# Kernel tuning notes

Hardware: AMD Instinct MI355X
Metric: run time of the kernel (lower is better)

## Reference

```python
import jax, jax.numpy as jnp
import numpy as np

# ---- static configuration matching init_kwargs ----
SEG = 2                 # segment_size hard-coded in the module
MUL0, MUL1 = 256, 128   # irreps = 256x0e + 128x1o
G = MUL1 // SEG         # 64 groups of 2x1o
INV_DIM = MUL0 + 3 * G  # 448 scalars (0e) after concat with channel_mix
N_IRREPS = INV_DIM + MUL1 + G + 3 * G  # 832 total irreps after regroup
N_NODES = 32768
EPS = 1e-6
_ISQ2 = 1.0 / np.sqrt(2.0)
_ISQ3 = 1.0 / np.sqrt(3.0)
_ISQ6 = 1.0 / np.sqrt(6.0)


def _cg_l2(a, b):
    """CG contraction 1 x 1 -> 2: project a_i b_j onto the 5 orthonormal
    symmetric-traceless basis matrices. a, b: [..., 3] -> [..., 5]."""
    ax, ay, az = a[..., 0], a[..., 1], a[..., 2]
    bx, by, bz = b[..., 0], b[..., 1], b[..., 2]
    return jnp.stack([
        (ax * by + ay * bx) * _ISQ2,
        (ax * bz + az * bx) * _ISQ2,
        (ay * bz + az * by) * _ISQ2,
        (ax * bx - ay * by) * _ISQ2,
        (2 * az * bz - ax * bx - ay * by) * _ISQ6,
    ], axis=-1)


def setup_inputs() -> dict:
    key = jax.random.key(0)
    k = jax.random.split(key, 5)
    return {
        "x":   jax.random.normal(k[0], (N_NODES, MUL0 + 3 * MUL1), dtype=jnp.float32),
        "W1":  jax.random.normal(k[1], (INV_DIM, INV_DIM),   dtype=jnp.float32),
        "W2":  jax.random.normal(k[2], (INV_DIM, N_IRREPS),  dtype=jnp.float32),
        "Wl0": jax.random.normal(k[3], (INV_DIM, MUL0),      dtype=jnp.float32),
        "Wl1": jax.random.normal(k[4], (MUL1, MUL1),         dtype=jnp.float32),
    }


def reference(x, W1, W2, Wl0, Wl1):
    N = x.shape[0]
    dt = x.dtype
    s = x[:, :MUL0]                       # [N, 256]  0e features
    v = x[:, MUL0:].reshape(N, MUL1, 3)   # [N, 128, 3]  1o features

    # ---- segmented tensor_square: groups of 2x1o -> 3x0e + 1x1e + 3x2e ----
    vg = v.reshape(N, G, SEG, 3)
    a, b = vg[:, :, 0], vg[:, :, 1]
    sq2 = jnp.sqrt(jnp.asarray(2.0, dt))
    # 0e: symmetric pairs (0,0), (0,1)*sqrt2, (1,1); CG = delta_ij/sqrt3
    t0 = jnp.stack([(a * a).sum(-1), sq2 * (a * b).sum(-1), (b * b).sum(-1)], -1) * _ISQ3  # [N,G,3]
    # 1e: antisymmetric pair (0,1); CG = eps/sqrt2, pair factor sqrt2 -> plain cross
    t1 = jnp.cross(a, b)                                                                   # [N,G,3]
    # 2e: symmetric pairs
    t2 = jnp.stack([_cg_l2(a, a), sq2 * _cg_l2(a, b), _cg_l2(b, b)], 2)                    # [N,G,3,5]

    # ---- concatenate + regroup (axis_to_mul folds group axis into mul) ----
    s_all = jnp.concatenate([s, t0.reshape(N, 3 * G)], -1)  # [N,448]  448x0e
    v1o = v                                                 # [N,128,3] 128x1o
    v1e = t1                                                # [N,64,3]   64x1e
    v2e = t2.reshape(N, 3 * G, 5)                           # [N,192,5] 192x2e

    # ---- gating MLP on invariants: [448 -> 448 (silu) -> 832] ----
    inv_fan = jnp.sqrt(jnp.asarray(INV_DIM, dt))
    h = jax.nn.silu(s_all @ W1 / inv_fan)
    gates = h @ W2 / inv_fan                                # [N, 832] one scalar per irrep
    g0, g1o, g1e, g2e = jnp.split(gates, [INV_DIM, INV_DIM + MUL1, INV_DIM + MUL1 + G], -1)
    s_all = s_all * g0
    v1o = v1o * g1o[..., None]
    # (v1e * g1e, v2e * g2e are dropped by the Linear below -> omitted, output identical)
    del v1e, v2e, g1e, g2e

    # ---- e3nn Linear to output irreps 256x0e + 128x1o (1e, 2e have no output) ----
    o0 = s_all @ Wl0 / inv_fan                                                   # [N,256]
    o1 = jnp.einsum('nmi,mk->nki', v1o, Wl1) / jnp.sqrt(jnp.asarray(MUL1, dt))   # [N,128,3]

    # ---- equivariant layer norm ----
    mu = o0.mean(-1, keepdims=True)
    var = ((o0 - mu) ** 2).mean(-1, keepdims=True)
    o0 = (o0 - mu) * jax.lax.rsqrt(var + EPS)
    rms = jnp.sqrt((o1 ** 2).mean((-2, -1), keepdims=True) + EPS)
    o1 = o1 / rms

    return jnp.concatenate([o0, o1.reshape(N, 3 * MUL1)], -1)  # [N, 640]
```

## Files before the change

kernel.cpp:

```cpp
#include <hip/hip_runtime.h>
#include <math.h>


typedef float floatx4 __attribute__((ext_vector_type(4)));
typedef __bf16 bf16x8 __attribute__((ext_vector_type(8)));

__device__ __forceinline__ unsigned short f2bf(float f) {
    union { float f; unsigned u; } v; v.f = f;
    unsigned r = v.u + 0x7FFFu + ((v.u >> 16) & 1u);
    return (unsigned short)(r >> 16);
}
__device__ __forceinline__ float bf2f(unsigned short u) {
    union { unsigned u; float f; } v; v.u = ((unsigned)u) << 16; return v.f;
}

__global__ __launch_bounds__(256) void wcast_kernel(
    const float* __restrict__ W1, const float* __restrict__ W2,
    const float* __restrict__ Wl0, const float* __restrict__ Wl1,
    unsigned short* __restrict__ W1F, unsigned short* __restrict__ W2F,
    unsigned short* __restrict__ Wl0F, unsigned short* __restrict__ Wl1F)
{
    int idx = blockIdx.x * 256 + threadIdx.x;
    if (idx < 200704) {
        int e = idx & 7, lane = (idx >> 3) & 63, r2 = idx >> 9;
        int kc = r2 % 14, t = r2 / 14;
        int col = t * 16 + (lane & 15);
        int k   = kc * 32 + (lane >> 4) * 8 + e;
        W1F[idx] = f2bf(W1[k * 448 + col]);
    } else if (idx < 458752) {
        int r = idx - 200704;
        int e = r & 7, lane = (r >> 3) & 63, r2 = r >> 9;
        int kc = r2 % 14, t = r2 / 14;
        int col = t * 16 + (lane & 15);
        int k   = kc * 32 + (lane >> 4) * 8 + e;
        W2F[r] = f2bf(W2[k * 832 + col]);
    } else if (idx < 573440) {
        int r = idx - 458752;
        int e = r & 7, lane = (r >> 3) & 63, r2 = r >> 9;
        int kc = r2 % 14, t = r2 / 14;
        int col = t * 16 + (lane & 15);
        int k   = kc * 32 + (lane >> 4) * 8 + e;
        Wl0F[r] = f2bf(Wl0[k * 256 + col]);
    } else if (idx < 589824) {
        int r = idx - 573440;
        int e = r & 7, lane = (r >> 3) & 63, r2 = r >> 9;
        int kc = r2 % 4, t = r2 / 4;
        int col = t * 16 + (lane & 15);
        int k   = kc * 32 + (lane >> 4) * 8 + e;
        Wl1F[r] = f2bf(Wl1[k * 128 + col]);
    }
}

template<int MT, int NT, int NKC>
__device__ __forceinline__ void gemm_stream(
    const unsigned short* __restrict__ BF, const int tileBase,
    const unsigned short* __restrict__ Albs, const int ldsA, const int rowBase,
    const int lane, const int l15, const int quad, const int wn,
    floatx4 (&acc)[MT][NT])
{
    const unsigned short* bp[NT];
    #pragma unroll
    for (int j = 0; j < NT; ++j)
        bp[j] = BF + ((size_t)(tileBase + wn + 4 * j) * NKC * 64 + lane) * 8;
    #pragma unroll
    for (int kc = 0; kc < NKC; ++kc) {
        bf16x8 af[MT];
        #pragma unroll
        for (int mt = 0; mt < MT; ++mt)
            af[mt] = *(const bf16x8*)&Albs[(rowBase + mt * 16 + l15) * ldsA + kc * 32 + quad * 8];
        #pragma unroll
        for (int j = 0; j < NT; ++j) {
            bf16x8 bfv = *(const bf16x8*)(bp[j] + kc * 512);
            #pragma unroll
            for (int mt = 0; mt < MT; ++mt)
                acc[mt][j] = __builtin_amdgcn_mfma_f32_16x16x32_bf16(af[mt], bfv, acc[mt][j], 0, 0, 0);
        }
    }
}

__global__ __launch_bounds__(512, 2) void fused_kernel(
    const float* __restrict__ x,
    const unsigned short* __restrict__ W1F,
    const unsigned short* __restrict__ W2F,
    const unsigned short* __restrict__ Wl0F,
    const unsigned short* __restrict__ Wl1F,
    float* __restrict__ out)
{
    __shared__ unsigned short sa[64][472];
    __shared__ unsigned short hb[64][472];
    __shared__ unsigned short g1[64][128];
    __shared__ float red[832];

    const int tid  = threadIdx.x;
    const int lane = tid & 63;
    const int l15  = lane & 15;
    const int quad = lane >> 4;
    const int w    = tid >> 6;
    const int wm   = w >> 2;
    const int wn   = w & 3;
    const int n0   = blockIdx.x * 64;

    const float s1 = 0.047245559f;
    const float s2 = 0.088388348f;

    {
        const int r = tid >> 3, sub = tid & 7;
        const float* xr = x + (size_t)(n0 + r) * 640;
        #pragma unroll
        for (int i = 0; i < 8; ++i) {
            int c4 = i * 8 + sub;
            float4 f = *(const float4*)(xr + c4 * 4);
            uint2 p;
            p.x = (unsigned)f2bf(f.x) | ((unsigned)f2bf(f.y) << 16);
            p.y = (unsigned)f2bf(f.z) | ((unsigned)f2bf(f.w) << 16);
            *(uint2*)&sa[r][c4 * 4] = p;
        }
        const float* xv = xr + 256;
        #pragma unroll
        for (int i = 0; i < 8; ++i) {
            int g = i * 8 + sub;
            const float2* vg = (const float2*)(xv + 6 * g);
            float2 p0 = vg[0], p1 = vg[1], p2 = vg[2];
            float ax = p0.x, ay = p0.y, az = p1.x;
            float bx = p1.y, by = p2.x, bz = p2.y;
            float aa = ax*ax + ay*ay + az*az;
            float ab = ax*bx + ay*by + az*bz;
            float bb = bx*bx + by*by + bz*bz;
            const float ISQ3 = 0.57735026918962576f;
            const float SQ2  = 1.41421356237309505f;
            sa[r][256 + 3*g]     = f2bf(aa * ISQ3);
            sa[r][256 + 3*g + 1] = f2bf(SQ2 * ab * ISQ3);
            sa[r][256 + 3*g + 2] = f2bf(bb * ISQ3);
        }
    }
    __syncthreads();

    {
        floatx4 acc[2][7] = {};
        gemm_stream<2,7,14>(W1F, 0, &sa[0][0], 472, wm*32, lane, l15, quad, wn, acc);
        #pragma unroll
        for (int j = 0; j < 7; ++j) {
            const int col = (wn + 4*j) * 16 + l15;
            #pragma unroll
            for (int mt = 0; mt < 2; ++mt)
                #pragma unroll
                for (int r = 0; r < 4; ++r) {
                    float v = acc[mt][j][r] * s1;
                    v = v / (1.f + __expf(-v));
                    hb[wm*32 + mt*16 + quad*4 + r][col] = f2bf(v);
                }
        }
    }
    __syncthreads();

    {
        floatx4 acc[2][9] = {};
        gemm_stream<2,9,14>(W2F, 0, &hb[0][0], 472, wm*32, lane, l15, quad, wn, acc);
        __syncthreads();
        #pragma unroll
        for (int j = 0; j < 9; ++j) {
            const int colb = (wn + 4*j) * 16;
            if (colb < 448) {
                const int col = colb + l15;
                #pragma unroll
                for (int mt = 0; mt < 2; ++mt)
                    #pragma unroll
                    for (int r = 0; r < 4; ++r) {
                        const int row = wm*32 + mt*16 + quad*4 + r;
                        hb[row][col] = f2bf(bf2f(sa[row][col]) * (acc[mt][j][r] * s1));
                    }
            } else {
                const int m = colb - 448 + l15;
                #pragma unroll
                for (int mt = 0; mt < 2; ++mt)
                    #pragma unroll
                    for (int r = 0; r < 4; ++r) {
                        const int row = wm*32 + mt*16 + quad*4 + r;
                        g1[row][m] = f2bf(acc[mt][j][r] * s1);
                    }
            }
        }
    }
    __syncthreads();

    {
        unsigned short* wmp = &sa[0][0];
        #pragma unroll
        for (int e0 = 0; e0 < 6144; e0 += 512) {
            int e4 = e0 + tid;
            int rl = e4 / 96;
            int c4 = (e4 - rl * 96) * 4;
            float4 xv = *(const float4*)(x + (size_t)(n0 + rl) * 640 + 256 + c4);
            float vv[4] = {xv.x, xv.y, xv.z, xv.w};
            #pragma unroll
            for (int d = 0; d < 4; ++d) {
                int rem = c4 + d;
                int m = rem / 3;
                int i = rem - 3 * m;
                wmp[(rl * 3 + i) * 136 + m] = f2bf(vv[d] * bf2f(g1[rl][m]));
            }
        }
    }
    __syncthreads();

    {
        floatx4 acc[2][4] = {};
        gemm_stream<2,4,14>(Wl0F, 0, &hb[0][0], 472, wm*32, lane, l15, quad, wn, acc);
        #pragma unroll
        for (int mt = 0; mt < 2; ++mt)
            #pragma unroll
            for (int r = 0; r < 4; ++r) {
                float sv = 0.f, sq = 0.f;
                #pragma unroll
                for (int j = 0; j < 4; ++j) {
                    float v = acc[mt][j][r] * s1;
                    sv += v; sq += v * v;
                }
                #pragma unroll
                for (int off = 1; off <= 8; off <<= 1) {
                    sv += __shfl_xor(sv, off);
                    sq += __shfl_xor(sq, off);
                }
                if (l15 == 0) {
                    const int row = wm*32 + mt*16 + quad*4 + r;
                    red[row * 8 + wn * 2]     = sv;
                    red[row * 8 + wn * 2 + 1] = sq;
                }
            }
        __syncthreads();
        #pragma unroll
        for (int mt = 0; mt < 2; ++mt)
            #pragma unroll
            for (int r = 0; r < 4; ++r) {
                const int row = wm*32 + mt*16 + quad*4 + r;
                float ts = red[row*8+0] + red[row*8+2] + red[row*8+4] + red[row*8+6];
                float tq = red[row*8+1] + red[row*8+3] + red[row*8+5] + red[row*8+7];
                float mu  = ts * (1.f/256.f);
                float var = tq * (1.f/256.f) - mu * mu;
                float rln = rsqrtf(var + 1e-6f);
                float* orow = out + (size_t)(n0 + row) * 640;
                #pragma unroll
                for (int j = 0; j < 4; ++j)
                    orow[(wn + 4*j)*16 + l15] = (acc[mt][j][r] * s1 - mu) * rln;
            }
    }
    __syncthreads();

    {
        floatx4 acc[6][2] = {};
        gemm_stream<6,2,4>(Wl1F, 0, &sa[0][0] , 136, wm*96, lane, l15, quad, wn, acc);
        #pragma unroll
        for (int mt = 0; mt < 6; ++mt)
            #pragma unroll
            for (int r = 0; r < 4; ++r) {
                float q = 0.f;
                #pragma unroll
                for (int j = 0; j < 2; ++j) {
                    float v = acc[mt][j][r] * s2;
                    q += v * v;
                }
                #pragma unroll
                for (int off = 1; off <= 8; off <<= 1) q += __shfl_xor(q, off);
                if (l15 == 0) {
                    const int row = wm*96 + mt*16 + quad*4 + r;
                    red[row * 4 + wn] = q;
                }
            }
        __syncthreads();
        if (tid < 64) {
            float s = 0.f;
            #pragma unroll
            for (int rr = 0; rr < 3; ++rr)
                #pragma unroll
                for (int w2 = 0; w2 < 4; ++w2)
                    s += red[(tid*3 + rr) * 4 + w2];
            red[768 + tid] = rsqrtf(s * (1.f/384.f) + 1e-6f);
        }
        __syncthreads();
        #pragma unroll
        for (int mt = 0; mt < 6; ++mt)
            #pragma unroll
            for (int r = 0; r < 4; ++r) {
                const int row = wm*96 + mt*16 + quad*4 + r;
                const int nl  = row / 3;
                const int i   = row - 3 * nl;
                const float rms = red[768 + nl];
                float* op = out + (size_t)(n0 + nl) * 640 + 256 + i;
                #pragma unroll
                for (int j = 0; j < 2; ++j)
                    op[3 * ((wn + 4*j)*16 + l15)] = acc[mt][j][r] * s2 * rms;
            }
    }
}

extern "C" void kernel_launch(void* const* d_in, const int* in_sizes, int n_in,
                              void* d_out, int out_size, void* d_ws, size_t ws_size,
                              hipStream_t stream) {
    const float* x   = (const float*)d_in[0];
    const float* W1  = (const float*)d_in[1];
    const float* W2  = (const float*)d_in[2];
    const float* Wl0 = (const float*)d_in[3];
    const float* Wl1 = (const float*)d_in[4];
    float* out = (float*)d_out;
    char* ws = (char*)d_ws;

    unsigned short* W1F  = (unsigned short*)(ws + 0);
    unsigned short* W2F  = (unsigned short*)(ws + 401408);
    unsigned short* Wl0F = (unsigned short*)(ws + 917504);
    unsigned short* Wl1F = (unsigned short*)(ws + 1146880);

    wcast_kernel<<<dim3(2304), dim3(256), 0, stream>>>(W1, W2, Wl0, Wl1, W1F, W2F, Wl0F, Wl1F);
    fused_kernel<<<dim3(512), dim3(512), 0, stream>>>(x, W1F, W2F, Wl0F, Wl1F, out);
}
```

Baseline: 259.4 us.

## Halve node tile to 32 rows for higher occupancy and vectorize weight cast

```diff
diff --git a/kernel.cpp b/kernel.cpp
--- a/kernel.cpp
+++ b/kernel.cpp
@@ -21,34 +21,29 @@
     unsigned short* __restrict__ Wl0F, unsigned short* __restrict__ Wl1F)
 {
     int idx = blockIdx.x * 256 + threadIdx.x;
-    if (idx < 200704) {
-        int e = idx & 7, lane = (idx >> 3) & 63, r2 = idx >> 9;
-        int kc = r2 % 14, t = r2 / 14;
-        int col = t * 16 + (lane & 15);
-        int k   = kc * 32 + (lane >> 4) * 8 + e;
-        W1F[idx] = f2bf(W1[k * 448 + col]);
-    } else if (idx < 458752) {
-        int r = idx - 200704;
-        int e = r & 7, lane = (r >> 3) & 63, r2 = r >> 9;
-        int kc = r2 % 14, t = r2 / 14;
-        int col = t * 16 + (lane & 15);
-        int k   = kc * 32 + (lane >> 4) * 8 + e;
-        W2F[r] = f2bf(W2[k * 832 + col]);
-    } else if (idx < 573440) {
-        int r = idx - 458752;
-        int e = r & 7, lane = (r >> 3) & 63, r2 = r >> 9;
-        int kc = r2 % 14, t = r2 / 14;
-        int col = t * 16 + (lane & 15);
-        int k   = kc * 32 + (lane >> 4) * 8 + e;
-        Wl0F[r] = f2bf(Wl0[k * 256 + col]);
-    } else if (idx < 589824) {
-        int r = idx - 573440;
-        int e = r & 7, lane = (r >> 3) & 63, r2 = r >> 9;
-        int kc = r2 % 4, t = r2 / 4;
-        int col = t * 16 + (lane & 15);
-        int k   = kc * 32 + (lane >> 4) * 8 + e;
-        Wl1F[r] = f2bf(Wl1[k * 128 + col]);
-    }
+    const float* src; unsigned short* dst;
+    int T, NKC, ld, k, rem;
+    if (idx < 25088) {
+        k = idx / 56; rem = idx % 56; src = W1; dst = W1F; T = 28; NKC = 14; ld = 448;
+    } else if (idx < 57344) {
+        int r = idx - 25088;
+        k = r / 72; rem = r % 72; src = W2; dst = W2F; T = 36; NKC = 14; ld = 832;
+    } else if (idx < 71680) {
+        int r = idx - 57344;
+        k = r / 32; rem = r % 32; src = Wl0; dst = Wl0F; T = 16; NKC = 14; ld = 256;
+    } else if (idx < 73728) {
+        int r = idx - 71680;
+        k = r / 16; rem = r % 16; src = Wl1; dst = Wl1F; T = 8; NKC = 4; ld = 128;
+    } else return;
+    int t = rem >> 1, c8 = rem & 1;
+    const float* s = src + (size_t)k * ld + t * 16 + c8 * 8;
+    float4 f0 = *(const float4*)s;
+    float4 f1 = *(const float4*)(s + 4);
+    int kc = k >> 5, q = (k >> 3) & 3, e = k & 7;
+    unsigned short* base = dst + ((size_t)(t * NKC + kc) * 64 + q * 16 + c8 * 8) * 8 + e;
+    float v[8] = {f0.x, f0.y, f0.z, f0.w, f1.x, f1.y, f1.z, f1.w};
+    #pragma unroll
+    for (int d = 0; d < 8; ++d) base[d * 8] = f2bf(v[d]);
 }
 
 template<int MT, int NT, int NKC>
@@ -78,7 +73,7 @@
     }
 }
 
-__global__ __launch_bounds__(512, 2) void fused_kernel(
+__global__ __launch_bounds__(512, 4) void fused_kernel(
     const float* __restrict__ x,
     const unsigned short* __restrict__ W1F,
     const unsigned short* __restrict__ W2F,
@@ -86,10 +81,10 @@
     const unsigned short* __restrict__ Wl1F,
     float* __restrict__ out)
 {
-    __shared__ unsigned short sa[64][472];
-    __shared__ unsigned short hb[64][472];
-    __shared__ unsigned short g1[64][128];
-    __shared__ float red[832];
+    __shared__ unsigned short sa[32][472];
+    __shared__ unsigned short hb[32][472];
+    __shared__ unsigned short g1[32][128];
+    __shared__ float red[416];
 
     const int tid  = threadIdx.x;
     const int lane = tid & 63;
@@ -98,17 +93,17 @@
     const int w    = tid >> 6;
     const int wm   = w >> 2;
     const int wn   = w & 3;
-    const int n0   = blockIdx.x * 64;
+    const int n0   = blockIdx.x * 32;
 
     const float s1 = 0.047245559f;
     const float s2 = 0.088388348f;
 
     {
-        const int r = tid >> 3, sub = tid & 7;
+        const int r = tid >> 4, sub = tid & 15;
         const float* xr = x + (size_t)(n0 + r) * 640;
         #pragma unroll
-        for (int i = 0; i < 8; ++i) {
-            int c4 = i * 8 + sub;
+        for (int i = 0; i < 4; ++i) {
+            int c4 = i * 16 + sub;
             float4 f = *(const float4*)(xr + c4 * 4);
             uint2 p;
             p.x = (unsigned)f2bf(f.x) | ((unsigned)f2bf(f.y) << 16);
@@ -117,8 +112,8 @@
         }
         const float* xv = xr + 256;
         #pragma unroll
-        for (int i = 0; i < 8; ++i) {
-            int g = i * 8 + sub;
+        for (int i = 0; i < 4; ++i) {
+            int g = i * 16 + sub;
             const float2* vg = (const float2*)(xv + 6 * g);
             float2 p0 = vg[0], p1 = vg[1], p2 = vg[2];
             float ax = p0.x, ay = p0.y, az = p1.x;
@@ -136,26 +131,24 @@
     __syncthreads();
 
     {
-        floatx4 acc[2][7] = {};
-        gemm_stream<2,7,14>(W1F, 0, &sa[0][0], 472, wm*32, lane, l15, quad, wn, acc);
+        floatx4 acc[1][7] = {};
+        gemm_stream<1,7,14>(W1F, 0, &sa[0][0], 472, wm*16, lane, l15, quad, wn, acc);
         #pragma unroll
         for (int j = 0; j < 7; ++j) {
             const int col = (wn + 4*j) * 16 + l15;
             #pragma unroll
-            for (int mt = 0; mt < 2; ++mt)
-                #pragma unroll
-                for (int r = 0; r < 4; ++r) {
-                    float v = acc[mt][j][r] * s1;
-                    v = v / (1.f + __expf(-v));
-                    hb[wm*32 + mt*16 + quad*4 + r][col] = f2bf(v);
-                }
-        }
-    }
-    __syncthreads();
-
-    {
-        floatx4 acc[2][9] = {};
-        gemm_stream<2,9,14>(W2F, 0, &hb[0][0], 472, wm*32, lane, l15, quad, wn, acc);
+            for (int r = 0; r < 4; ++r) {
+                float v = acc[0][j][r] * s1;
+                v = v / (1.f + __expf(-v));
+                hb[wm*16 + quad*4 + r][col] = f2bf(v);
+            }
+        }
+    }
+    __syncthreads();
+
+    {
+        floatx4 acc[1][9] = {};
+        gemm_stream<1,9,14>(W2F, 0, &hb[0][0], 472, wm*16, lane, l15, quad, wn, acc);
         __syncthreads();
         #pragma unroll
         for (int j = 0; j < 9; ++j) {
@@ -163,21 +156,17 @@
             if (colb < 448) {
                 const int col = colb + l15;
                 #pragma unroll
-                for (int mt = 0; mt < 2; ++mt)
-                    #pragma unroll
-                    for (int r = 0; r < 4; ++r) {
-                        const int row = wm*32 + mt*16 + quad*4 + r;
-                        hb[row][col] = f2bf(bf2f(sa[row][col]) * (acc[mt][j][r] * s1));
-                    }
+                for (int r = 0; r < 4; ++r) {
+                    const int row = wm*16 + quad*4 + r;
+                    hb[row][col] = f2bf(bf2f(sa[row][col]) * (acc[0][j][r] * s1));
+                }
             } else {
                 const int m = colb - 448 + l15;
                 #pragma unroll
-                for (int mt = 0; mt < 2; ++mt)
-                    #pragma unroll
-                    for (int r = 0; r < 4; ++r) {
-                        const int row = wm*32 + mt*16 + quad*4 + r;
-                        g1[row][m] = f2bf(acc[mt][j][r] * s1);
-                    }
+                for (int r = 0; r < 4; ++r) {
+                    const int row = wm*16 + quad*4 + r;
+                    g1[row][m] = f2bf(acc[0][j][r] * s1);
+                }
             }
         }
     }
@@ -186,7 +175,7 @@
     {
         unsigned short* wmp = &sa[0][0];
         #pragma unroll
-        for (int e0 = 0; e0 < 6144; e0 += 512) {
+        for (int e0 = 0; e0 < 3072; e0 += 512) {
             int e4 = e0 + tid;
             int rl = e4 / 96;
             int c4 = (e4 - rl * 96) * 4;
@@ -204,53 +193,49 @@
     __syncthreads();
 
     {
-        floatx4 acc[2][4] = {};
-        gemm_stream<2,4,14>(Wl0F, 0, &hb[0][0], 472, wm*32, lane, l15, quad, wn, acc);
-        #pragma unroll
-        for (int mt = 0; mt < 2; ++mt)
-            #pragma unroll
-            for (int r = 0; r < 4; ++r) {
-                float sv = 0.f, sq = 0.f;
-                #pragma unroll
-                for (int j = 0; j < 4; ++j) {
-                    float v = acc[mt][j][r] * s1;
-                    sv += v; sq += v * v;
-                }
-                #pragma unroll
-                for (int off = 1; off <= 8; off <<= 1) {
-                    sv += __shfl_xor(sv, off);
-                    sq += __shfl_xor(sq, off);
-                }
-                if (l15 == 0) {
-                    const int row = wm*32 + mt*16 + quad*4 + r;
-                    red[row * 8 + wn * 2]     = sv;
-                    red[row * 8 + wn * 2 + 1] = sq;
-                }
-            }
-        __syncthreads();
-        #pragma unroll
-        for (int mt = 0; mt < 2; ++mt)
-            #pragma unroll
-            for (int r = 0; r < 4; ++r) {
-                const int row = wm*32 + mt*16 + quad*4 + r;
-                float ts = red[row*8+0] + red[row*8+2] + red[row*8+4] + red[row*8+6];
-                float tq = red[row*8+1] + red[row*8+3] + red[row*8+5] + red[row*8+7];
-                float mu  = ts * (1.f/256.f);
-                float var = tq * (1.f/256.f) - mu * mu;
-                float rln = rsqrtf(var + 1e-6f);
-                float* orow = out + (size_t)(n0 + row) * 640;
-                #pragma unroll
-                for (int j = 0; j < 4; ++j)
-                    orow[(wn + 4*j)*16 + l15] = (acc[mt][j][r] * s1 - mu) * rln;
-            }
-    }
-    __syncthreads();
-
-    {
-        floatx4 acc[6][2] = {};
-        gemm_stream<6,2,4>(Wl1F, 0, &sa[0][0] , 136, wm*96, lane, l15, quad, wn, acc);
-        #pragma unroll
-        for (int mt = 0; mt < 6; ++mt)
+        floatx4 acc[1][4] = {};
+        gemm_stream<1,4,14>(Wl0F, 0, &hb[0][0], 472, wm*16, lane, l15, quad, wn, acc);
+        #pragma unroll
+        for (int r = 0; r < 4; ++r) {
+            float sv = 0.f, sq = 0.f;
+            #pragma unroll
+            for (int j = 0; j < 4; ++j) {
+                float v = acc[0][j][r] * s1;
+                sv += v; sq += v * v;
+            }
+            #pragma unroll
+            for (int off = 1; off <= 8; off <<= 1) {
+                sv += __shfl_xor(sv, off);
+                sq += __shfl_xor(sq, off);
+            }
+            if (l15 == 0) {
+                const int row = wm*16 + quad*4 + r;
+                red[row * 8 + wn * 2]     = sv;
+                red[row * 8 + wn * 2 + 1] = sq;
+            }
+        }
+        __syncthreads();
+        #pragma unroll
+        for (int r = 0; r < 4; ++r) {
+            const int row = wm*16 + quad*4 + r;
+            float ts = red[row*8+0] + red[row*8+2] + red[row*8+4] + red[row*8+6];
+            float tq = red[row*8+1] + red[row*8+3] + red[row*8+5] + red[row*8+7];
+            float mu  = ts * (1.f/256.f);
+            float var = tq * (1.f/256.f) - mu * mu;
+            float rln = rsqrtf(var + 1e-6f);
+            float* orow = out + (size_t)(n0 + row) * 640;
+            #pragma unroll
+            for (int j = 0; j < 4; ++j)
+                orow[(wn + 4*j)*16 + l15] = (acc[0][j][r] * s1 - mu) * rln;
+        }
+    }
+    __syncthreads();
+
+    {
+        floatx4 acc[3][2] = {};
+        gemm_stream<3,2,4>(Wl1F, 0, &sa[0][0] , 136, wm*48, lane, l15, quad, wn, acc);
+        #pragma unroll
+        for (int mt = 0; mt < 3; ++mt)
             #pragma unroll
             for (int r = 0; r < 4; ++r) {
                 float q = 0.f;
@@ -262,29 +247,29 @@
                 #pragma unroll
                 for (int off = 1; off <= 8; off <<= 1) q += __shfl_xor(q, off);
                 if (l15 == 0) {
-                    const int row = wm*96 + mt*16 + quad*4 + r;
+                    const int row = wm*48 + mt*16 + quad*4 + r;
                     red[row * 4 + wn] = q;
                 }
             }
         __syncthreads();
-        if (tid < 64) {
+        if (tid < 32) {
             float s = 0.f;
             #pragma unroll
             for (int rr = 0; rr < 3; ++rr)
                 #pragma unroll
                 for (int w2 = 0; w2 < 4; ++w2)
                     s += red[(tid*3 + rr) * 4 + w2];
-            red[768 + tid] = rsqrtf(s * (1.f/384.f) + 1e-6f);
-        }
-        __syncthreads();
-        #pragma unroll
-        for (int mt = 0; mt < 6; ++mt)
+            red[384 + tid] = rsqrtf(s * (1.f/384.f) + 1e-6f);
+        }
+        __syncthreads();
+        #pragma unroll
+        for (int mt = 0; mt < 3; ++mt)
             #pragma unroll
             for (int r = 0; r < 4; ++r) {
-                const int row = wm*96 + mt*16 + quad*4 + r;
+                const int row = wm*48 + mt*16 + quad*4 + r;
                 const int nl  = row / 3;
                 const int i   = row - 3 * nl;
-                const float rms = red[768 + nl];
+                const float rms = red[384 + nl];
                 float* op = out + (size_t)(n0 + nl) * 640 + 256 + i;
                 #pragma unroll
                 for (int j = 0; j < 2; ++j)
@@ -309,6 +294,6 @@
     unsigned short* Wl0F = (unsigned short*)(ws + 917504);
     unsigned short* Wl1F = (unsigned short*)(ws + 1146880);
 
-    wcast_kernel<<<dim3(2304), dim3(256), 0, stream>>>(W1, W2, Wl0, Wl1, W1F, W2F, Wl0F, Wl1F);
-    fused_kernel<<<dim3(512), dim3(512), 0, stream>>>(x, W1F, W2F, Wl0F, Wl1F, out);
-}
+    wcast_kernel<<<dim3(288), dim3(256), 0, stream>>>(W1, W2, Wl0, Wl1, W1F, W2F, Wl0F, Wl1F);
+    fused_kernel<<<dim3(1024), dim3(512), 0, stream>>>(x, W1F, W2F, Wl0F, Wl1F, out);
+}
```

New measurement: 298.7 us. 15.2% more time.

## Retile fused GEMMs so each wave covers all 64 rows and fewer columns

Applied to the files above, without the earlier changes.

```diff
diff --git a/kernel.cpp b/kernel.cpp
--- a/kernel.cpp
+++ b/kernel.cpp
@@ -6,9 +6,8 @@
 typedef __bf16 bf16x8 __attribute__((ext_vector_type(8)));
 
 __device__ __forceinline__ unsigned short f2bf(float f) {
-    union { float f; unsigned u; } v; v.f = f;
-    unsigned r = v.u + 0x7FFFu + ((v.u >> 16) & 1u);
-    return (unsigned short)(r >> 16);
+    __bf16 h = (__bf16)f;
+    return __builtin_bit_cast(unsigned short, h);
 }
 __device__ __forceinline__ float bf2f(unsigned short u) {
     union { unsigned u; float f; } v; v.u = ((unsigned)u) << 16; return v.f;
@@ -21,39 +20,39 @@
     unsigned short* __restrict__ Wl0F, unsigned short* __restrict__ Wl1F)
 {
     int idx = blockIdx.x * 256 + threadIdx.x;
-    if (idx < 200704) {
-        int e = idx & 7, lane = (idx >> 3) & 63, r2 = idx >> 9;
-        int kc = r2 % 14, t = r2 / 14;
-        int col = t * 16 + (lane & 15);
-        int k   = kc * 32 + (lane >> 4) * 8 + e;
-        W1F[idx] = f2bf(W1[k * 448 + col]);
-    } else if (idx < 458752) {
-        int r = idx - 200704;
-        int e = r & 7, lane = (r >> 3) & 63, r2 = r >> 9;
-        int kc = r2 % 14, t = r2 / 14;
-        int col = t * 16 + (lane & 15);
-        int k   = kc * 32 + (lane >> 4) * 8 + e;
-        W2F[r] = f2bf(W2[k * 832 + col]);
-    } else if (idx < 573440) {
-        int r = idx - 458752;
-        int e = r & 7, lane = (r >> 3) & 63, r2 = r >> 9;
-        int kc = r2 % 14, t = r2 / 14;
-        int col = t * 16 + (lane & 15);
-        int k   = kc * 32 + (lane >> 4) * 8 + e;
-        Wl0F[r] = f2bf(Wl0[k * 256 + col]);
-    } else if (idx < 589824) {
-        int r = idx - 573440;
-        int e = r & 7, lane = (r >> 3) & 63, r2 = r >> 9;
-        int kc = r2 % 4, t = r2 / 4;
-        int col = t * 16 + (lane & 15);
-        int k   = kc * 32 + (lane >> 4) * 8 + e;
-        Wl1F[r] = f2bf(Wl1[k * 128 + col]);
-    }
+    const float* src; unsigned short* dst;
+    int NKC, ld, colTrue, k, rem;
+    if (idx < 28672) {
+        k = idx / 64; rem = idx % 64; src = W1; dst = W1F; NKC = 14; ld = 448; colTrue = 448;
+    } else if (idx < 64512) {
+        int r = idx - 28672;
+        k = r / 80; rem = r % 80; src = W2; dst = W2F; NKC = 14; ld = 832; colTrue = 576;
+    } else if (idx < 78848) {
+        int r = idx - 64512;
+        k = r / 32; rem = r % 32; src = Wl0; dst = Wl0F; NKC = 14; ld = 256; colTrue = 256;
+    } else if (idx < 80896) {
+        int r = idx - 78848;
+        k = r / 16; rem = r % 16; src = Wl1; dst = Wl1F; NKC = 4; ld = 128; colTrue = 128;
+    } else return;
+    int t = rem >> 1, c8 = rem & 1;
+    int col0 = t * 16 + c8 * 8;
+    float v[8] = {0.f, 0.f, 0.f, 0.f, 0.f, 0.f, 0.f, 0.f};
+    if (col0 < colTrue) {
+        const float* s = src + (size_t)k * ld + col0;
+        float4 f0 = *(const float4*)s;
+        float4 f1 = *(const float4*)(s + 4);
+        v[0]=f0.x; v[1]=f0.y; v[2]=f0.z; v[3]=f0.w;
+        v[4]=f1.x; v[5]=f1.y; v[6]=f1.z; v[7]=f1.w;
+    }
+    int kc = k >> 5, q = (k >> 3) & 3, e = k & 7;
+    unsigned short* base = dst + ((size_t)(t * NKC + kc) * 64 + q * 16 + c8 * 8) * 8 + e;
+    #pragma unroll
+    for (int d = 0; d < 8; ++d) base[d * 8] = f2bf(v[d]);
 }
 
 template<int MT, int NT, int NKC>
 __device__ __forceinline__ void gemm_stream(
-    const unsigned short* __restrict__ BF, const int tileBase,
+    const unsigned short* __restrict__ BF,
     const unsigned short* __restrict__ Albs, const int ldsA, const int rowBase,
     const int lane, const int l15, const int quad, const int wn,
     floatx4 (&acc)[MT][NT])
@@ -61,7 +60,7 @@
     const unsigned short* bp[NT];
     #pragma unroll
     for (int j = 0; j < NT; ++j)
-        bp[j] = BF + ((size_t)(tileBase + wn + 4 * j) * NKC * 64 + lane) * 8;
+        bp[j] = BF + ((size_t)(wn + 8 * j) * NKC * 64 + lane) * 8;
     #pragma unroll
     for (int kc = 0; kc < NKC; ++kc) {
         bf16x8 af[MT];
@@ -89,15 +88,13 @@
     __shared__ unsigned short sa[64][472];
     __shared__ unsigned short hb[64][472];
     __shared__ unsigned short g1[64][128];
-    __shared__ float red[832];
+    __shared__ float red[1600];
 
     const int tid  = threadIdx.x;
     const int lane = tid & 63;
     const int l15  = lane & 15;
     const int quad = lane >> 4;
-    const int w    = tid >> 6;
-    const int wm   = w >> 2;
-    const int wn   = w & 3;
+    const int wn   = tid >> 6;
     const int n0   = blockIdx.x * 64;
 
     const float s1 = 0.047245559f;
@@ -110,10 +107,8 @@
         for (int i = 0; i < 8; ++i) {
             int c4 = i * 8 + sub;
             float4 f = *(const float4*)(xr + c4 * 4);
-            uint2 p;
-            p.x = (unsigned)f2bf(f.x) | ((unsigned)f2bf(f.y) << 16);
-            p.y = (unsigned)f2bf(f.z) | ((unsigned)f2bf(f.w) << 16);
-            *(uint2*)&sa[r][c4 * 4] = p;
+            unsigned short* o = &sa[r][c4 * 4];
+            o[0] = f2bf(f.x); o[1] = f2bf(f.y); o[2] = f2bf(f.z); o[3] = f2bf(f.w);
         }
         const float* xv = xr + 256;
         #pragma unroll
@@ -136,46 +131,49 @@
     __syncthreads();
 
     {
-        floatx4 acc[2][7] = {};
-        gemm_stream<2,7,14>(W1F, 0, &sa[0][0], 472, wm*32, lane, l15, quad, wn, acc);
-        #pragma unroll
-        for (int j = 0; j < 7; ++j) {
-            const int col = (wn + 4*j) * 16 + l15;
-            #pragma unroll
-            for (int mt = 0; mt < 2; ++mt)
-                #pragma unroll
-                for (int r = 0; r < 4; ++r) {
-                    float v = acc[mt][j][r] * s1;
-                    v = v / (1.f + __expf(-v));
-                    hb[wm*32 + mt*16 + quad*4 + r][col] = f2bf(v);
-                }
-        }
-    }
-    __syncthreads();
-
-    {
-        floatx4 acc[2][9] = {};
-        gemm_stream<2,9,14>(W2F, 0, &hb[0][0], 472, wm*32, lane, l15, quad, wn, acc);
-        __syncthreads();
-        #pragma unroll
-        for (int j = 0; j < 9; ++j) {
-            const int colb = (wn + 4*j) * 16;
+        floatx4 acc[4][4] = {};
+        gemm_stream<4,4,14>(W1F, &sa[0][0], 472, 0, lane, l15, quad, wn, acc);
+        #pragma unroll
+        for (int j = 0; j < 4; ++j) {
+            const int colb = (wn + 8*j) * 16;
             if (colb < 448) {
                 const int col = colb + l15;
                 #pragma unroll
-                for (int mt = 0; mt < 2; ++mt)
+                for (int mt = 0; mt < 4; ++mt)
                     #pragma unroll
                     for (int r = 0; r < 4; ++r) {
-                        const int row = wm*32 + mt*16 + quad*4 + r;
+                        float v = acc[mt][j][r] * s1;
+                        v = v / (1.f + __expf(-v));
+                        hb[mt*16 + quad*4 + r][col] = f2bf(v);
+                    }
+            }
+        }
+    }
+    __syncthreads();
+
+    {
+        floatx4 acc[4][5] = {};
+        gemm_stream<4,5,14>(W2F, &hb[0][0], 472, 0, lane, l15, quad, wn, acc);
+        __syncthreads();
+        #pragma unroll
+        for (int j = 0; j < 5; ++j) {
+            const int colb = (wn + 8*j) * 16;
+            if (colb < 448) {
+                const int col = colb + l15;
+                #pragma unroll
+                for (int mt = 0; mt < 4; ++mt)
+                    #pragma unroll
+                    for (int r = 0; r < 4; ++r) {
+                        const int row = mt*16 + quad*4 + r;
                         hb[row][col] = f2bf(bf2f(sa[row][col]) * (acc[mt][j][r] * s1));
                     }
-            } else {
+            } else if (colb < 576) {
                 const int m = colb - 448 + l15;
                 #pragma unroll
-                for (int mt = 0; mt < 2; ++mt)
+                for (int mt = 0; mt < 4; ++mt)
                     #pragma unroll
                     for (int r = 0; r < 4; ++r) {
-                        const int row = wm*32 + mt*16 + quad*4 + r;
+                        const int row = mt*16 + quad*4 + r;
                         g1[row][m] = f2bf(acc[mt][j][r] * s1);
                     }
             }
@@ -204,15 +202,15 @@
     __syncthreads();
 
     {
-        floatx4 acc[2][4] = {};
-        gemm_stream<2,4,14>(Wl0F, 0, &hb[0][0], 472, wm*32, lane, l15, quad, wn, acc);
-        #pragma unroll
-        for (int mt = 0; mt < 2; ++mt)
+        floatx4 acc[4][2] = {};
+        gemm_stream<4,2,14>(Wl0F, &hb[0][0], 472, 0, lane, l15, quad, wn, acc);
+        #pragma unroll
+        for (int mt = 0; mt < 4; ++mt)
             #pragma unroll
             for (int r = 0; r < 4; ++r) {
                 float sv = 0.f, sq = 0.f;
                 #pragma unroll
-                for (int j = 0; j < 4; ++j) {
+                for (int j = 0; j < 2; ++j) {
                     float v = acc[mt][j][r] * s1;
                     sv += v; sq += v * v;
                 }
@@ -222,48 +220,48 @@
                     sq += __shfl_xor(sq, off);
                 }
                 if (l15 == 0) {
-                    const int row = wm*32 + mt*16 + quad*4 + r;
-                    red[row * 8 + wn * 2]     = sv;
-                    red[row * 8 + wn * 2 + 1] = sq;
+                    const int row = mt*16 + quad*4 + r;
+                    red[row * 8 + wn]       = sv;
+                    red[512 + row * 8 + wn] = sq;
                 }
             }
         __syncthreads();
         #pragma unroll
-        for (int mt = 0; mt < 2; ++mt)
+        for (int mt = 0; mt < 4; ++mt)
             #pragma unroll
             for (int r = 0; r < 4; ++r) {
-                const int row = wm*32 + mt*16 + quad*4 + r;
-                float ts = red[row*8+0] + red[row*8+2] + red[row*8+4] + red[row*8+6];
-                float tq = red[row*8+1] + red[row*8+3] + red[row*8+5] + red[row*8+7];
+                const int row = mt*16 + quad*4 + r;
+                float ts = 0.f, tq = 0.f;
+                #pragma unroll
+                for (int w2 = 0; w2 < 8; ++w2) {
+                    ts += red[row*8 + w2];
+                    tq += red[512 + row*8 + w2];
+                }
                 float mu  = ts * (1.f/256.f);
                 float var = tq * (1.f/256.f) - mu * mu;
                 float rln = rsqrtf(var + 1e-6f);
                 float* orow = out + (size_t)(n0 + row) * 640;
                 #pragma unroll
-                for (int j = 0; j < 4; ++j)
-                    orow[(wn + 4*j)*16 + l15] = (acc[mt][j][r] * s1 - mu) * rln;
-            }
-    }
-    __syncthreads();
-
-    {
-        floatx4 acc[6][2] = {};
-        gemm_stream<6,2,4>(Wl1F, 0, &sa[0][0] , 136, wm*96, lane, l15, quad, wn, acc);
-        #pragma unroll
-        for (int mt = 0; mt < 6; ++mt)
+                for (int j = 0; j < 2; ++j)
+                    orow[(wn + 8*j)*16 + l15] = (acc[mt][j][r] * s1 - mu) * rln;
+            }
+    }
+    __syncthreads();
+
+    {
+        floatx4 acc[12][1] = {};
+        gemm_stream<12,1,4>(Wl1F, &sa[0][0] , 136, 0, lane, l15, quad, wn, acc);
+        #pragma unroll
+        for (int mt = 0; mt < 12; ++mt)
             #pragma unroll
             for (int r = 0; r < 4; ++r) {
-                float q = 0.f;
-                #pragma unroll
-                for (int j = 0; j < 2; ++j) {
-                    float v = acc[mt][j][r] * s2;
-                    q += v * v;
-                }
+                float v = acc[mt][0][r] * s2;
+                float q = v * v;
                 #pragma unroll
                 for (int off = 1; off <= 8; off <<= 1) q += __shfl_xor(q, off);
                 if (l15 == 0) {
-                    const int row = wm*96 + mt*16 + quad*4 + r;
-                    red[row * 4 + wn] = q;
+                    const int row = mt*16 + quad*4 + r;
+                    red[row * 8 + wn] = q;
                 }
             }
         __syncthreads();
@@ -272,23 +270,21 @@
             #pragma unroll
             for (int rr = 0; rr < 3; ++rr)
                 #pragma unroll
-                for (int w2 = 0; w2 < 4; ++w2)
-                    s += red[(tid*3 + rr) * 4 + w2];
-            red[768 + tid] = rsqrtf(s * (1.f/384.f) + 1e-6f);
+                for (int w2 = 0; w2 < 8; ++w2)
+                    s += red[(tid*3 + rr) * 8 + w2];
+            red[1536 + tid] = rsqrtf(s * (1.f/384.f) + 1e-6f);
         }
         __syncthreads();
         #pragma unroll
-        for (int mt = 0; mt < 6; ++mt)
+        for (int mt = 0; mt < 12; ++mt)
             #pragma unroll
             for (int r = 0; r < 4; ++r) {
-                const int row = wm*96 + mt*16 + quad*4 + r;
+                const int row = mt*16 + quad*4 + r;
                 const int nl  = row / 3;
                 const int i   = row - 3 * nl;
-                const float rms = red[768 + nl];
+                const float rms = red[1536 + nl];
                 float* op = out + (size_t)(n0 + nl) * 640 + 256 + i;
-                #pragma unroll
-                for (int j = 0; j < 2; ++j)
-                    op[3 * ((wn + 4*j)*16 + l15)] = acc[mt][j][r] * s2 * rms;
+                op[3 * (wn*16 + l15)] = acc[mt][0][r] * s2 * rms;
             }
     }
 }
@@ -305,10 +301,10 @@
     char* ws = (char*)d_ws;
 
     unsigned short* W1F  = (unsigned short*)(ws + 0);
-    unsigned short* W2F  = (unsigned short*)(ws + 401408);
-    unsigned short* Wl0F = (unsigned short*)(ws + 917504);
-    unsigned short* Wl1F = (unsigned short*)(ws + 1146880);
-
-    wcast_kernel<<<dim3(2304), dim3(256), 0, stream>>>(W1, W2, Wl0, Wl1, W1F, W2F, Wl0F, Wl1F);
+    unsigned short* W2F  = (unsigned short*)(ws + 458752);
+    unsigned short* Wl0F = (unsigned short*)(ws + 1032192);
+    unsigned short* Wl1F = (unsigned short*)(ws + 1261568);
+
+    wcast_kernel<<<dim3(316), dim3(256), 0, stream>>>(W1, W2, Wl0, Wl1, W1F, W2F, Wl0F, Wl1F);
     fused_kernel<<<dim3(512), dim3(512), 0, stream>>>(x, W1F, W2F, Wl0F, Wl1F, out);
 }
```

Result: faster. 248.3 us (-4.3%).
